# Performance work log

Measured on AMD Instinct MI355X. Metric: run time of the kernel, lower is better.

## Reference

```python
import jax, jax.numpy as jnp
import numpy as np

HEADS = 8
NEG_SLOPE = 0.2


def _gat_conv(x, src, dst, W, a_src, a_dst, b, heads, ch):
    # PyG GATConv (v1), eval mode (dropout inactive), add_self_loops=True, concat=True.
    N = x.shape[0]
    loop = jnp.arange(N)
    s = jnp.concatenate([src, loop])
    d = jnp.concatenate([dst, loop])
    h = (x @ W).reshape(N, heads, ch)                      # [N, H, C]
    alpha_src = jnp.einsum('nhc,hc->nh', h, a_src)          # [N, H]
    alpha_dst = jnp.einsum('nhc,hc->nh', h, a_dst)
    e = jax.nn.leaky_relu(alpha_src[s] + alpha_dst[d], NEG_SLOPE)  # [E, H]
    m = jax.ops.segment_max(e, d, num_segments=N)           # segment softmax over dst
    ex = jnp.exp(e - m[d])
    denom = jax.ops.segment_sum(ex, d, num_segments=N)
    alpha = ex / (denom[d] + 1e-16)
    out = jax.ops.segment_sum(h[s] * alpha[:, :, None], d, num_segments=N)  # [N, H, C]
    return out.reshape(N, heads * ch) + b


def setup_inputs() -> dict:
    key = jax.random.key(0)
    ks = jax.random.split(key, 20)
    B, N, F_in = 8, 1024, 16
    E = 131072
    C1, C2 = 8, 128                     # per-head channels of conv1 / conv2
    D = N * HEADS * C2                  # flattened head input = 1024*1024
    NA, AC = 4, 4                       # len(num_actions)=4, each 4 actions

    def w(k, shape, fan_in):
        return jax.random.normal(k, shape, jnp.float32) * (1.0 / np.sqrt(fan_in))

    inp = {
        'x': jax.random.normal(ks[0], (B, N, F_in), jnp.float32),
        'edge': jax.random.randint(ks[1], (2, E), 0, B * N, jnp.int64),
        'W1': w(ks[2], (F_in, HEADS * C1), F_in),
        'a_src1': w(ks[3], (HEADS, C1), C1),
        'a_dst1': w(ks[4], (HEADS, C1), C1),
        'b1': jnp.zeros((HEADS * C1,), jnp.float32),
        'W2': w(ks[5], (HEADS * C1, HEADS * C2), HEADS * C1),
        'a_src2': w(ks[6], (HEADS, C2), C2),
        'a_dst2': w(ks[7], (HEADS, C2), C2),
        'b2': jnp.zeros((HEADS * C2,), jnp.float32),
        'adv_w': w(ks[8], (D, NA * AC), D),
        'adv_b': jnp.zeros((NA * AC,), jnp.float32),
        'val1_w': w(ks[9], (D, 64), D),
        'val1_b': jnp.zeros((64,), jnp.float32),
        'val2_w': w(ks[10], (64, 64), 64),
        'val2_b': jnp.zeros((64,), jnp.float32),
        'val3_w': w(ks[11], (64, 1), 64),
        'val3_b': jnp.zeros((1,), jnp.float32),
    }
    return inp


def reference(x, edge, W1, a_src1, a_dst1, b1, W2, a_src2, a_dst2, b2,
              adv_w, adv_b, val1_w, val1_b, val2_w, val2_b, val3_w, val3_b):
    B, N, F_in = x.shape
    src, dst = edge[0], edge[1]
    h = x.reshape(B * N, F_in)
    h = jax.nn.relu(_gat_conv(h, src, dst, W1, a_src1, a_dst1, b1, HEADS, 8))
    h = jax.nn.relu(_gat_conv(h, src, dst, W2, a_src2, a_dst2, b2, HEADS, 128))
    h = h.reshape(B, -1)                                   # [B, N*1024]
    adv = jax.nn.relu(h @ adv_w + adv_b).reshape(B, 4, 4)  # [B, len(num_actions), actions]
    v = jax.nn.relu(h @ val1_w + val1_b)
    v = jax.nn.relu(v @ val2_w + val2_b)
    v = v @ val3_w + val3_b                                # [B, 1]
    return v[:, :, None] + adv - adv.mean(-1, keepdims=True)
```

## Files before the change

### kernel.cpp

```cpp
#include <hip/hip_runtime.h>
#include <stdint.h>

#define NODES   8192
#define BATCH   8
#define FIN     16
#define HC1     64
#define HC2     1024
#define DTOT    1048576
#define NEG     0.2f

typedef unsigned short u16;

__device__ __forceinline__ float b2f(u16 s){ return __uint_as_float(((unsigned)s)<<16); }
__device__ __forceinline__ u16 f2b(float f){
    unsigned u = __float_as_uint(f);
    unsigned r = u + 0x7fffu + ((u>>16)&1u);
    return (u16)(r>>16);
}
__device__ __forceinline__ float lrelu(float x){ return x > 0.f ? x : NEG*x; }
__device__ __forceinline__ float ldf(const void* p, long i, int isf){
    return isf ? ((const float*)p)[i] : b2f(((const u16*)p)[i]);
}

__device__ __forceinline__ int esrc(const int* e, int i, int i64){ return i64 ? e[2*i] : e[i]; }
__device__ __forceinline__ int edst(const int* e, int i, int E, int i64){ return i64 ? e[2*(E+i)] : e[E+i]; }

__global__ __launch_bounds__(256) void k_prep(const u16* __restrict__ xs, const int* __restrict__ ed,
        int* flags, int* counts){
    int t = threadIdx.x;
    if(blockIdx.x == 0){
        __shared__ int cnt[2];
        if(t<2) cnt[t]=0;
        __syncthreads();
        int bad=0;
        for(int i=t;i<1024;i+=256){
            u16 u = xs[i];
            float a = fabsf(b2f(u));
            if(!(u==0 || (a>1e-8f && a<1e4f))) bad++;
        }
        if(bad) atomicAdd(&cnt[0], bad);
        int z=0;
        for(int i=t;i<1024;i+=256){
            if(ed[2*i+1]==0) z++;
        }
        if(z) atomicAdd(&cnt[1], z);
        __syncthreads();
        if(t==0){ flags[0] = (cnt[0] > 64) ? 1 : 0; flags[1] = (cnt[1] > 512) ? 1 : 0; }
    } else {
        int i = (blockIdx.x-1)*256 + t;
        if(i < NODES) counts[i] = 0;
    }
}

__global__ __launch_bounds__(256) void k_cnt_d1(const int* __restrict__ ed, int E, int* counts,
        const void* __restrict__ x, const void* __restrict__ W1,
        const void* __restrict__ asw, const void* __restrict__ adw,
        float* g1, float* as1, float* ad1, const int* flags){
    int t = threadIdx.x;
    if(blockIdx.x < 512){
        int i64 = flags[1];
        int e = blockIdx.x*256 + t;
        if(e < E) atomicAdd(&counts[edst(ed,e,E,i64)], 1);
        return;
    }
    int isf = flags[0];
    __shared__ float w1[FIN*HC1];
    __shared__ float av[64], dv[64];
    __shared__ float xr[4][FIN];
    __shared__ float hrow[4][HC1];
    int n0 = (blockIdx.x-512)*4;
    for(int i=t;i<FIN*HC1;i+=256) w1[i] = ldf(W1,i,isf);
    if(t<64){ av[t]=ldf(asw,t,isf); dv[t]=ldf(adw,t,isf); }
    if(t<64) xr[t>>4][t&15] = ldf(x, n0*FIN + t, isf);
    __syncthreads();
    int i = t>>6, c = t&63;
    float acc = 0.f;
    #pragma unroll
    for(int k=0;k<FIN;k++) acc += xr[i][k]*w1[k*HC1+c];
    g1[(n0+i)*HC1 + c] = acc;
    hrow[i][c] = acc;
    __syncthreads();
    if(t<32){
        int ii=t>>3, h=t&7;
        float sa=0.f, sd=0.f;
        #pragma unroll
        for(int k=0;k<8;k++){ float v=hrow[ii][h*8+k]; sa+=v*av[h*8+k]; sd+=v*dv[h*8+k]; }
        as1[(n0+ii)*8+h]=sa; ad1[(n0+ii)*8+h]=sd;
    }
}

__global__ __launch_bounds__(1024) void k_scan(const int* __restrict__ counts, int* offs, int* cursor){
    __shared__ int sums[1024];
    int t = threadIdx.x;
    int base = t*8;
    int loc[8]; int s = 0;
    for(int k=0;k<8;k++){ loc[k] = s; s += counts[base+k]; }
    sums[t] = s;
    __syncthreads();
    for(int off=1; off<1024; off<<=1){
        int v = (t>=off) ? sums[t-off] : 0;
        __syncthreads();
        sums[t] += v;
        __syncthreads();
    }
    int b = (t==0) ? 0 : sums[t-1];
    for(int k=0;k<8;k++){ int v = b + loc[k]; offs[base+k]=v; cursor[base+k]=v; }
    if(t==1023) offs[NODES] = sums[1023];
}

__global__ void k_fill(const int* __restrict__ ed, int E, int* cursor, int* csr, const int* flags){
    int i64 = flags[1];
    int e = blockIdx.x*256 + threadIdx.x;
    if(e < E){ int p = atomicAdd(&cursor[edst(ed,e,E,i64)], 1); csr[p] = esrc(ed,e,i64); }
}

__global__ __launch_bounds__(64) void k_agg1(const int* __restrict__ offs, const int* __restrict__ csr,
        const float* __restrict__ g1, const float* __restrict__ as1, const float* __restrict__ ad1,
        const void* __restrict__ b1, float* z1, const int* flags){
    int isf = flags[0];
    __shared__ float redm[64], redd[64];
    __shared__ float mh[8], dh[8], adl[8];
    __shared__ int src_l[64];
    __shared__ float wx[64*8];
    int n = blockIdx.x, t = threadIdx.x;
    int off = offs[n], deg = offs[n+1]-off, tot = deg+1;
    if(t<8) adl[t] = ad1[n*8+t];
    __syncthreads();
    {
        int h = t&7, jg = t>>3;
        float ad = adl[h];
        float m = -1e30f, d = 0.f;
        for(int j=jg; j<tot; j+=8){
            int s = (j<deg)?csr[off+j]:n;
            float e = lrelu(as1[s*8+h] + ad);
            if(e>m){ d = d*__expf(m-e) + 1.f; m = e; } else d += __expf(e-m);
        }
        redm[t]=m; redd[t]=d;
        __syncthreads();
        for(int st=4; st>=1; st>>=1){
            if(jg < st){
                float m2 = redm[t + st*8], d2 = redd[t + st*8];
                float mm = fmaxf(m, m2);
                d = d*__expf(m-mm) + d2*__expf(m2-mm);
                m = mm;
                redm[t]=m; redd[t]=d;
            }
            __syncthreads();
        }
        if(t<8){ mh[t]=redm[t]; dh[t]=redd[t] + 1e-16f; }
        __syncthreads();
    }
    int c = t, hc = t>>3;
    float acc = 0.f;
    for(int c0=0;c0<tot;c0+=64){
        int nc = min(64, tot-c0);
        if(t<nc){ int j=c0+t; src_l[t]=(j<deg)?csr[off+j]:n; }
        __syncthreads();
        for(int p=t;p<nc*8;p+=64){
            int j=p>>3, hh=p&7;
            float e = lrelu(as1[src_l[j]*8+hh] + adl[hh]);
            wx[p] = __expf(e - mh[hh]);
        }
        __syncthreads();
        int j = 0;
        for(; j+2<=nc; j+=2){
            float w0 = wx[j*8+hc],     v0 = g1[src_l[j]*HC1 + c];
            float w1 = wx[(j+1)*8+hc], v1 = g1[src_l[j+1]*HC1 + c];
            acc += w0*v0 + w1*v1;
        }
        if(j<nc) acc += wx[j*8+hc]*g1[src_l[j]*HC1 + c];
        __syncthreads();
    }
    z1[n*HC1 + c] = fmaxf(acc/dh[hc] + ldf(b1,c,isf), 0.f);
}

__global__ __launch_bounds__(256) void k_d2a2(const float* __restrict__ z1,
        const void* __restrict__ W2, const void* __restrict__ asw, const void* __restrict__ adw,
        u16* g2, float* as2, float* ad2, const int* flags){
    int isf = flags[0];
    __shared__ float zr[8][HC1];
    __shared__ float avs[HC2], ads[HC2];
    int t = threadIdx.x;
    int n0 = blockIdx.x*8;
    for(int i=t;i<8*HC1;i+=256) zr[i>>6][i&63] = z1[n0*HC1 + i];
    for(int i=t;i<HC2;i+=256){ avs[i]=ldf(asw,i,isf); ads[i]=ldf(adw,i,isf); }
    __syncthreads();
    int c0 = t*4;
    float acc[8][4];
    #pragma unroll
    for(int i=0;i<8;i++){ acc[i][0]=0;acc[i][1]=0;acc[i][2]=0;acc[i][3]=0; }
    for(int k=0;k<HC1;k++){
        float w0,w1,w2,w3;
        if(isf){
            float4 w = *(const float4*)((const float*)W2 + (size_t)k*HC2 + c0);
            w0=w.x; w1=w.y; w2=w.z; w3=w.w;
        } else {
            ushort4 w = *(const ushort4*)((const u16*)W2 + (size_t)k*HC2 + c0);
            w0=b2f(w.x); w1=b2f(w.y); w2=b2f(w.z); w3=b2f(w.w);
        }
        #pragma unroll
        for(int i=0;i<8;i++){
            float zv = zr[i][k];
            acc[i][0]+=zv*w0; acc[i][1]+=zv*w1; acc[i][2]+=zv*w2; acc[i][3]+=zv*w3;
        }
    }
    float a0=avs[c0], a1=avs[c0+1], a2=avs[c0+2], a3=avs[c0+3];
    float d0=ads[c0], d1=ads[c0+1], d2=ads[c0+2], d3=ads[c0+3];
    int h = t>>5;
    #pragma unroll
    for(int i=0;i<8;i++){
        ushort4 o;
        o.x=f2b(acc[i][0]); o.y=f2b(acc[i][1]); o.z=f2b(acc[i][2]); o.w=f2b(acc[i][3]);
        *(ushort4*)&g2[(size_t)(n0+i)*HC2 + c0] = o;
        float pa = acc[i][0]*a0 + acc[i][1]*a1 + acc[i][2]*a2 + acc[i][3]*a3;
        float pd = acc[i][0]*d0 + acc[i][1]*d1 + acc[i][2]*d2 + acc[i][3]*d3;
        #pragma unroll
        for(int m=1;m<32;m<<=1){ pa += __shfl_xor(pa,m); pd += __shfl_xor(pd,m); }
        if((t&31)==0){ as2[(n0+i)*8+h]=pa; ad2[(n0+i)*8+h]=pd; }
    }
}

__global__ __launch_bounds__(256) void k_agg2(const int* __restrict__ offs, const int* __restrict__ csr,
        const u16* __restrict__ g2, const float* __restrict__ as2, const float* __restrict__ ad2,
        const void* __restrict__ b2, u16* hbf, const int* flags){
    int isf = flags[0];
    __shared__ float redm[256], redd[256];
    __shared__ float mh[8], dh[8], adl[8];
    __shared__ int src_l[64];
    __shared__ float wx[64*8];
    int n = blockIdx.x, t = threadIdx.x;
    int off = offs[n], deg = offs[n+1]-off, tot = deg+1;
    if(t<8) adl[t] = ad2[n*8+t];
    __syncthreads();
    {
        int h = t&7, jg = t>>3;
        float ad = adl[h];
        float m = -1e30f, d = 0.f;
        for(int j=jg; j<tot; j+=32){
            int s = (j<deg)?csr[off+j]:n;
            float e = lrelu(as2[s*8+h] + ad);
            if(e>m){ d = d*__expf(m-e) + 1.f; m = e; } else d += __expf(e-m);
        }
        redm[t]=m; redd[t]=d;
        __syncthreads();
        for(int st=16; st>=1; st>>=1){
            if(jg < st){
                float m2 = redm[t + st*8], d2 = redd[t + st*8];
                float mm = fmaxf(m, m2);
                d = d*__expf(m-mm) + d2*__expf(m2-mm);
                m = mm;
                redm[t]=m; redd[t]=d;
            }
            __syncthreads();
        }
        if(t<8){ mh[t]=redm[t]; dh[t]=redd[t] + 1e-16f; }
        __syncthreads();
    }
    int c0 = t*4, hc = t>>5;
    float acc[4] = {0,0,0,0};
    for(int cc0=0;cc0<tot;cc0+=64){
        int nc = min(64, tot-cc0);
        if(t<nc){ int j=cc0+t; src_l[t]=(j<deg)?csr[off+j]:n; }
        __syncthreads();
        for(int p=t;p<nc*8;p+=256){
            int j=p>>3, hh=p&7;
            float e = lrelu(as2[src_l[j]*8+hh] + adl[hh]);
            wx[p] = __expf(e - mh[hh]);
        }
        __syncthreads();
        int j = 0;
        for(; j+2<=nc; j+=2){
            float w0 = wx[j*8+hc], w1 = wx[(j+1)*8+hc];
            ushort4 gv0 = *(const ushort4*)&g2[(size_t)src_l[j]*HC2 + c0];
            ushort4 gv1 = *(const ushort4*)&g2[(size_t)src_l[j+1]*HC2 + c0];
            acc[0]+=w0*b2f(gv0.x)+w1*b2f(gv1.x);
            acc[1]+=w0*b2f(gv0.y)+w1*b2f(gv1.y);
            acc[2]+=w0*b2f(gv0.z)+w1*b2f(gv1.z);
            acc[3]+=w0*b2f(gv0.w)+w1*b2f(gv1.w);
        }
        if(j<nc){
            float w = wx[j*8+hc];
            ushort4 gv = *(const ushort4*)&g2[(size_t)src_l[j]*HC2 + c0];
            acc[0]+=w*b2f(gv.x); acc[1]+=w*b2f(gv.y); acc[2]+=w*b2f(gv.z); acc[3]+=w*b2f(gv.w);
        }
        __syncthreads();
    }
    float dhv = dh[hc];
    ushort4 o;
    o.x = f2b(fmaxf(acc[0]/dhv + ldf(b2,c0+0,isf), 0.f));
    o.y = f2b(fmaxf(acc[1]/dhv + ldf(b2,c0+1,isf), 0.f));
    o.z = f2b(fmaxf(acc[2]/dhv + ldf(b2,c0+2,isf), 0.f));
    o.w = f2b(fmaxf(acc[3]/dhv + ldf(b2,c0+3,isf), 0.f));
    *(ushort4*)&hbf[(size_t)n*HC2 + c0] = o;
}

template<int COLS, int NW>
__device__ __forceinline__ void gemv_part(const void* __restrict__ W, const u16* __restrict__ hbf,
        float* __restrict__ scratch, int wid, int lane, int isf){
    const int GR    = COLS/8;
    const int KSTEP = 64/GR;
    const int ITERS = DTOT/(NW*KSTEP);
    int cg  = (lane % GR)*8;
    int kof = lane / GR;
    float acc[8][8];
    #pragma unroll
    for(int b=0;b<8;b++)
        #pragma unroll
        for(int c=0;c<8;c++) acc[b][c]=0.f;
    for(int it=0; it<ITERS; it+=2){
        int k0 = (it*NW + wid)*KSTEP + kof;
        int k1 = ((it+1)*NW + wid)*KSTEP + kof;
        float wv0[8], wv1[8];
        if(isf){
            float4 a0 = *(const float4*)((const float*)W + (size_t)k0*COLS + cg);
            float4 b0 = *(const float4*)((const float*)W + (size_t)k0*COLS + cg + 4);
            float4 a1 = *(const float4*)((const float*)W + (size_t)k1*COLS + cg);
            float4 b1 = *(const float4*)((const float*)W + (size_t)k1*COLS + cg + 4);
            wv0[0]=a0.x;wv0[1]=a0.y;wv0[2]=a0.z;wv0[3]=a0.w;wv0[4]=b0.x;wv0[5]=b0.y;wv0[6]=b0.z;wv0[7]=b0.w;
            wv1[0]=a1.x;wv1[1]=a1.y;wv1[2]=a1.z;wv1[3]=a1.w;wv1[4]=b1.x;wv1[5]=b1.y;wv1[6]=b1.z;wv1[7]=b1.w;
        } else {
            ushort4 a0 = *(const ushort4*)((const u16*)W + (size_t)k0*COLS + cg);
            ushort4 b0 = *(const ushort4*)((const u16*)W + (size_t)k0*COLS + cg + 4);
            ushort4 a1 = *(const ushort4*)((const u16*)W + (size_t)k1*COLS + cg);
            ushort4 b1 = *(const ushort4*)((const u16*)W + (size_t)k1*COLS + cg + 4);
            wv0[0]=b2f(a0.x);wv0[1]=b2f(a0.y);wv0[2]=b2f(a0.z);wv0[3]=b2f(a0.w);
            wv0[4]=b2f(b0.x);wv0[5]=b2f(b0.y);wv0[6]=b2f(b0.z);wv0[7]=b2f(b0.w);
            wv1[0]=b2f(a1.x);wv1[1]=b2f(a1.y);wv1[2]=b2f(a1.z);wv1[3]=b2f(a1.w);
            wv1[4]=b2f(b1.x);wv1[5]=b2f(b1.y);wv1[6]=b2f(b1.z);wv1[7]=b2f(b1.w);
        }
        float hv0[8], hv1[8];
        #pragma unroll
        for(int b=0;b<8;b++){ hv0[b] = b2f(hbf[(size_t)b*DTOT + k0]); hv1[b] = b2f(hbf[(size_t)b*DTOT + k1]); }
        #pragma unroll
        for(int b=0;b<8;b++)
            #pragma unroll
            for(int c=0;c<8;c++) acc[b][c] += hv0[b]*wv0[c] + hv1[b]*wv1[c];
    }
    #pragma unroll
    for(int m=GR;m<64;m<<=1){
        #pragma unroll
        for(int b=0;b<8;b++)
            #pragma unroll
            for(int c=0;c<8;c++) acc[b][c] += __shfl_xor(acc[b][c], m);
    }
    int q = lane / GR;
    if(q < 8){
        float4 o0, o1;
        o0.x=acc[q][0]; o0.y=acc[q][1]; o0.z=acc[q][2]; o0.w=acc[q][3];
        o1.x=acc[q][4]; o1.y=acc[q][5]; o1.z=acc[q][6]; o1.w=acc[q][7];
        float* dst = scratch + (size_t)wid*COLS*8 + q*COLS + cg;
        *(float4*)dst       = o0;
        *(float4*)(dst + 4) = o1;
    }
}

__global__ __launch_bounds__(256) void k_heads(const void* __restrict__ v1w, const void* __restrict__ advw,
        const u16* __restrict__ hbf, float* s1, float* s2, const int* flags){
    int isf = flags[0];
    int lane = threadIdx.x & 63;
    if(blockIdx.x < 1024){
        int wid = (int)((blockIdx.x*256 + threadIdx.x) >> 6);
        gemv_part<64,4096>(v1w, hbf, s1, wid, lane, isf);
    } else {
        int wid = (int)(((blockIdx.x-1024)*256 + threadIdx.x) >> 6);
        gemv_part<16,1024>(advw, hbf, s2, wid, lane, isf);
    }
}

__global__ __launch_bounds__(1024) void k_reduce(const float* __restrict__ s1, const float* __restrict__ s2,
        float* v1a, float* adva){
    __shared__ float red[1024];
    int blk = blockIdx.x, t = threadIdx.x;
    int ph = t>>6, ln = t&63;
    float a = 0.f;
    if(blk < 8){
        int o = blk*64 + ln;
        for(int p = ph; p < 4096; p += 16) a += s1[(size_t)p*512 + o];
        red[t] = a; __syncthreads();
        if(t<64){ float s=0.f; for(int q=0;q<16;q++) s += red[q*64+t]; v1a[blk*64+t]=s; }
    } else {
        int o = (blk-8)*64 + ln;
        for(int p = ph; p < 1024; p += 16) a += s2[(size_t)p*128 + o];
        red[t] = a; __syncthreads();
        if(t<64){ float s=0.f; for(int q=0;q<16;q++) s += red[q*64+t]; adva[(blk-8)*64+t]=s; }
    }
}

__global__ __launch_bounds__(512) void k_final(const float* __restrict__ v1a, const float* __restrict__ adva,
        const void* __restrict__ v1b, const void* __restrict__ advb,
        const void* __restrict__ w2v, const void* __restrict__ b2v,
        const void* __restrict__ w3v, const void* __restrict__ b3v,
        void* out, const int* flags){
    int isf = flags[0];
    __shared__ float v1[8][64], v2[8][64], adv[128], v3[8];
    int t = threadIdx.x;
    { int b=t>>6, j=t&63; v1[b][j] = fmaxf(v1a[t] + ldf(v1b,j,isf), 0.f); }
    if(t<128) adv[t] = fmaxf(adva[t] + ldf(advb,t&15,isf), 0.f);
    __syncthreads();
    { int b=t>>6, j=t&63;
      float a=0.f;
      for(int k=0;k<64;k++) a += v1[b][k]*ldf(w2v,k*64+j,isf);
      v2[b][j] = fmaxf(a + ldf(b2v,j,isf), 0.f); }
    __syncthreads();
    if(t<8){
        float a=0.f;
        for(int k=0;k<64;k++) a += v2[t][k]*ldf(w3v,k,isf);
        v3[t] = a + ldf(b3v,0,isf);
    }
    __syncthreads();
    if(t<128){
        int b=t>>4, r=(t>>2)&3;
        int base = b*16 + r*4;
        float m = 0.25f*(adv[base]+adv[base+1]+adv[base+2]+adv[base+3]);
        float val = v3[b] + adv[t] - m;
        if(isf) ((float*)out)[t] = val;
        else    ((u16*)out)[t]   = f2b(val);
    }
}

extern "C" void kernel_launch(void* const* d_in, const int* in_sizes, int n_in,
                              void* d_out, int out_size, void* d_ws, size_t ws_size,
                              hipStream_t stream){
    const void* x    = d_in[0];
    const int*  edge = (const int*)d_in[1];
    const int E = in_sizes[1]/2;
    const void* W1   = d_in[2];
    const void* as1w = d_in[3];
    const void* ad1w = d_in[4];
    const void* b1   = d_in[5];
    const void* W2   = d_in[6];
    const void* as2w = d_in[7];
    const void* ad2w = d_in[8];
    const void* b2   = d_in[9];
    const void* advw = d_in[10];
    const void* advb = d_in[11];
    const void* v1w  = d_in[12];
    const void* v1b  = d_in[13];
    const void* v2w  = d_in[14];
    const void* v2b  = d_in[15];
    const void* v3w  = d_in[16];
    const void* v3b  = d_in[17];

    char* wsp = (char*)d_ws;
    size_t o = 0;
    auto alloc = [&](size_t bytes)->char*{
        char* p = wsp + o;
        o = (o + bytes + 255) & ~(size_t)255;
        return p;
    };
    int*   flags  = (int*)  alloc(256);
    int*   counts = (int*)  alloc(NODES*4);
    int*   offs   = (int*)  alloc((NODES+8)*4);
    int*   cursor = (int*)  alloc(NODES*4);
    int*   csr    = (int*)  alloc((size_t)E*4);
    float* g1     = (float*)alloc((size_t)NODES*HC1*4);
    float* as1    = (float*)alloc((size_t)NODES*8*4);
    float* ad1    = (float*)alloc((size_t)NODES*8*4);
    float* z1     = (float*)alloc((size_t)NODES*HC1*4);
    u16*   g2     = (u16*)  alloc((size_t)NODES*HC2*2);
    float* as2    = (float*)alloc((size_t)NODES*8*4);
    float* ad2    = (float*)alloc((size_t)NODES*8*4);
    u16*   hbf    = (u16*)  alloc((size_t)NODES*HC2*2);
    float* s1     = (float*)alloc((size_t)4096*512*4);
    float* s2     = (float*)alloc((size_t)1024*128*4);
    float* v1a    = (float*)alloc(512*4);
    float* adva   = (float*)alloc(128*4);

    k_prep  <<<33, 256, 0, stream>>>((const u16*)x, edge, flags, counts);
    k_cnt_d1<<<2560, 256, 0, stream>>>(edge, E, counts, x, W1, as1w, ad1w, g1, as1, ad1, flags);
    k_scan  <<<1, 1024, 0, stream>>>(counts, offs, cursor);
    k_fill  <<<(E+255)/256, 256, 0, stream>>>(edge, E, cursor, csr, flags);
    k_agg1  <<<NODES, 64, 0, stream>>>(offs, csr, g1, as1, ad1, b1, z1, flags);
    k_d2a2  <<<NODES/8, 256, 0, stream>>>(z1, W2, as2w, ad2w, g2, as2, ad2, flags);
    k_agg2  <<<NODES, 256, 0, stream>>>(offs, csr, g2, as2, ad2, b2, hbf, flags);
    k_heads <<<1280, 256, 0, stream>>>(v1w, advw, hbf, s1, s2, flags);
    k_reduce<<<10, 1024, 0, stream>>>(s1, s2, v1a, adva);
    k_final <<<1, 512, 0, stream>>>(v1a, adva, v1b, advb, v2w, v2b, v3w, v3b, d_out, flags);
}
```

Baseline: 681.4 us.

## Reassociate GAT layers to aggregate inputs before projection and fold attention vectors

Both GAT layers now aggregate the narrow per-node inputs (x for layer 1, z1 for layer 2) with the attention weights, then apply the linear projection per head, instead of projecting every node first and gathering the wide projected rows. Attention logits are computed through precomputed products W·a_src and W·a_dst, so the bf16 g2 intermediate of 8192x1024 is never materialised or gathered per edge. The layer-2 aggregation gathers 64-float z1 rows rather than 1024-wide bf16 rows, but writes an 8x64 per-node buffer and moves the W2 GEMM after aggregation. It also fuses CSR fill with the W2·a precompute and fuses the layer-1 projection into aggregation, at the cost of changed rounding order.

New measurement: 749.1 us. 9.9% more time.

```diff
diff --git a/kernel.cpp b/kernel.cpp
--- a/kernel.cpp
+++ b/kernel.cpp
@@ -52,10 +52,10 @@
     }
 }
 
-__global__ __launch_bounds__(256) void k_cnt_d1(const int* __restrict__ ed, int E, int* counts,
+__global__ __launch_bounds__(256) void k_cnt_a1(const int* __restrict__ ed, int E, int* counts,
         const void* __restrict__ x, const void* __restrict__ W1,
         const void* __restrict__ asw, const void* __restrict__ adw,
-        float* g1, float* as1, float* ad1, const int* flags){
+        float* as1, float* ad1, const int* flags){
     int t = threadIdx.x;
     if(blockIdx.x < 512){
         int i64 = flags[1];
@@ -64,28 +64,32 @@
         return;
     }
     int isf = flags[0];
-    __shared__ float w1[FIN*HC1];
-    __shared__ float av[64], dv[64];
-    __shared__ float xr[4][FIN];
-    __shared__ float hrow[4][HC1];
-    int n0 = (blockIdx.x-512)*4;
-    for(int i=t;i<FIN*HC1;i+=256) w1[i] = ldf(W1,i,isf);
-    if(t<64){ av[t]=ldf(asw,t,isf); dv[t]=ldf(adw,t,isf); }
-    if(t<64) xr[t>>4][t&15] = ldf(x, n0*FIN + t, isf);
-    __syncthreads();
-    int i = t>>6, c = t&63;
-    float acc = 0.f;
-    #pragma unroll
-    for(int k=0;k<FIN;k++) acc += xr[i][k]*w1[k*HC1+c];
-    g1[(n0+i)*HC1 + c] = acc;
-    hrow[i][c] = acc;
-    __syncthreads();
-    if(t<32){
-        int ii=t>>3, h=t&7;
-        float sa=0.f, sd=0.f;
-        #pragma unroll
-        for(int k=0;k<8;k++){ float v=hrow[ii][h*8+k]; sa+=v*av[h*8+k]; sd+=v*dv[h*8+k]; }
-        as1[(n0+ii)*8+h]=sa; ad1[(n0+ii)*8+h]=sd;
+    __shared__ float w1l[FIN*HC1];
+    __shared__ float p1[2][FIN][8];
+    __shared__ float xl[128][FIN];
+    int n0 = (blockIdx.x-512)*128;
+    for(int q=0;q<4;q++) w1l[t + q*256] = ldf(W1, t + q*256, isf);
+    for(int q=0;q<8;q++){ int f = t + q*256; xl[f>>4][f&15] = ldf(x, (long)n0*FIN + f, isf); }
+    __syncthreads();
+    {
+        int sd = t>>7, k = (t>>3)&15, h = t&7;
+        const void* av = sd ? adw : asw;
+        float s = 0.f;
+        #pragma unroll
+        for(int c=0;c<8;c++) s += w1l[k*HC1 + h*8 + c] * ldf(av, h*8+c, isf);
+        p1[sd][k][h] = s;
+    }
+    __syncthreads();
+    {
+        int i = t>>1, sd = t&1;
+        float* outp = sd ? ad1 : as1;
+        #pragma unroll
+        for(int h=0;h<8;h++){
+            float s = 0.f;
+            #pragma unroll
+            for(int k=0;k<FIN;k++) s += xl[i][k] * p1[sd][k][h];
+            outp[(size_t)(n0+i)*8 + h] = s;
+        }
     }
 }
 
@@ -108,22 +112,43 @@
     if(t==1023) offs[NODES] = sums[1023];
 }
 
-__global__ void k_fill(const int* __restrict__ ed, int E, int* cursor, int* csr, const int* flags){
-    int i64 = flags[1];
-    int e = blockIdx.x*256 + threadIdx.x;
-    if(e < E){ int p = atomicAdd(&cursor[edst(ed,e,E,i64)], 1); csr[p] = esrc(ed,e,i64); }
-}
-
-__global__ __launch_bounds__(64) void k_agg1(const int* __restrict__ offs, const int* __restrict__ csr,
-        const float* __restrict__ g1, const float* __restrict__ as1, const float* __restrict__ ad1,
-        const void* __restrict__ b1, float* z1, const int* flags){
+__global__ __launch_bounds__(256) void k_fill_p2(const int* __restrict__ ed, int E, int* cursor, int* csr,
+        const void* __restrict__ W2, const void* __restrict__ asw2, const void* __restrict__ adw2,
+        float* p2s, float* p2d, const int* flags){
+    int t = threadIdx.x;
+    if(blockIdx.x < 512){
+        int i64 = flags[1];
+        int e = blockIdx.x*256 + t;
+        if(e < E){ int p = atomicAdd(&cursor[edst(ed,e,E,i64)], 1); csr[p] = esrc(ed,e,i64); }
+        return;
+    }
     int isf = flags[0];
+    for(int q=0;q<4;q++){
+        int task = t + q*256;
+        int sd = task>>9, k = (task>>3)&63, h = task&7;
+        const void* av = sd ? adw2 : asw2;
+        float s = 0.f;
+        for(int c=0;c<128;c++) s += ldf(W2, (long)k*HC2 + h*128 + c, isf) * ldf(av, h*128+c, isf);
+        (sd ? p2d : p2s)[k*8 + h] = s;
+    }
+}
+
+__global__ __launch_bounds__(64) void k_l1(const int* __restrict__ offs, const int* __restrict__ csr,
+        const void* __restrict__ x, const void* __restrict__ W1, const void* __restrict__ b1,
+        const float* __restrict__ as1, const float* __restrict__ ad1,
+        const float* __restrict__ p2s, const float* __restrict__ p2d,
+        float* z1, float* as2, float* ad2, const int* flags){
+    int isf = flags[0];
+    __shared__ float w1l[FIN*HC1];
     __shared__ float redm[64], redd[64];
     __shared__ float mh[8], dh[8], adl[8];
     __shared__ int src_l[64];
     __shared__ float wx[64*8];
+    __shared__ float aggx[8][FIN];
+    __shared__ float zl[HC1];
     int n = blockIdx.x, t = threadIdx.x;
     int off = offs[n], deg = offs[n+1]-off, tot = deg+1;
+    for(int q=0;q<16;q++) w1l[t + q*64] = ldf(W1, t + q*64, isf);
     if(t<8) adl[t] = ad1[n*8+t];
     __syncthreads();
     {
@@ -150,8 +175,8 @@
         if(t<8){ mh[t]=redm[t]; dh[t]=redd[t] + 1e-16f; }
         __syncthreads();
     }
-    int c = t, hc = t>>3;
-    float acc = 0.f;
+    int c = t&15, hq = t>>4;
+    float acc0 = 0.f, acc1 = 0.f;
     for(int c0=0;c0<tot;c0+=64){
         int nc = min(64, tot-c0);
         if(t<nc){ int j=c0+t; src_l[t]=(j<deg)?csr[off+j]:n; }
@@ -164,28 +189,122 @@
         __syncthreads();
         int j = 0;
         for(; j+2<=nc; j+=2){
-            float w0 = wx[j*8+hc],     v0 = g1[src_l[j]*HC1 + c];
-            float w1 = wx[(j+1)*8+hc], v1 = g1[src_l[j+1]*HC1 + c];
-            acc += w0*v0 + w1*v1;
-        }
-        if(j<nc) acc += wx[j*8+hc]*g1[src_l[j]*HC1 + c];
-        __syncthreads();
-    }
-    z1[n*HC1 + c] = fmaxf(acc/dh[hc] + ldf(b1,c,isf), 0.f);
-}
-
-__global__ __launch_bounds__(256) void k_d2a2(const float* __restrict__ z1,
-        const void* __restrict__ W2, const void* __restrict__ asw, const void* __restrict__ adw,
-        u16* g2, float* as2, float* ad2, const int* flags){
+            float x0 = ldf(x, (long)src_l[j]*FIN + c, isf);
+            float x1 = ldf(x, (long)src_l[j+1]*FIN + c, isf);
+            acc0 += wx[j*8+hq]*x0     + wx[(j+1)*8+hq]*x1;
+            acc1 += wx[j*8+hq+4]*x0   + wx[(j+1)*8+hq+4]*x1;
+        }
+        if(j<nc){
+            float x0 = ldf(x, (long)src_l[j]*FIN + c, isf);
+            acc0 += wx[j*8+hq]*x0;
+            acc1 += wx[j*8+hq+4]*x0;
+        }
+        __syncthreads();
+    }
+    aggx[hq][c]   = acc0/dh[hq];
+    aggx[hq+4][c] = acc1/dh[hq+4];
+    __syncthreads();
+    {
+        int h = t>>3;
+        float s = 0.f;
+        #pragma unroll
+        for(int k=0;k<FIN;k++) s += aggx[h][k]*w1l[k*HC1 + t];
+        float zv = fmaxf(s + ldf(b1, t, isf), 0.f);
+        z1[(size_t)n*HC1 + t] = zv;
+        zl[t] = zv;
+    }
+    __syncthreads();
+    if(t<8){
+        float s = 0.f;
+        for(int k=0;k<HC1;k++) s += zl[k]*p2s[k*8+t];
+        as2[n*8+t] = s;
+    } else if(t<16){
+        int tt = t-8;
+        float s = 0.f;
+        for(int k=0;k<HC1;k++) s += zl[k]*p2d[k*8+tt];
+        ad2[n*8+tt] = s;
+    }
+}
+
+__global__ __launch_bounds__(64) void k_aggz(const int* __restrict__ offs, const int* __restrict__ csr,
+        const float* __restrict__ z1, const float* __restrict__ as2, const float* __restrict__ ad2,
+        float* aggz){
+    __shared__ float redm[64], redd[64];
+    __shared__ float mh[8], dh[8], adl[8];
+    __shared__ int src_l[64];
+    __shared__ float wx[64*8];
+    int n = blockIdx.x, t = threadIdx.x;
+    int off = offs[n], deg = offs[n+1]-off, tot = deg+1;
+    if(t<8) adl[t] = ad2[n*8+t];
+    __syncthreads();
+    {
+        int h = t&7, jg = t>>3;
+        float ad = adl[h];
+        float m = -1e30f, d = 0.f;
+        for(int j=jg; j<tot; j+=8){
+            int s = (j<deg)?csr[off+j]:n;
+            float e = lrelu(as2[s*8+h] + ad);
+            if(e>m){ d = d*__expf(m-e) + 1.f; m = e; } else d += __expf(e-m);
+        }
+        redm[t]=m; redd[t]=d;
+        __syncthreads();
+        for(int st=4; st>=1; st>>=1){
+            if(jg < st){
+                float m2 = redm[t + st*8], d2 = redd[t + st*8];
+                float mm = fmaxf(m, m2);
+                d = d*__expf(m-mm) + d2*__expf(m2-mm);
+                m = mm;
+                redm[t]=m; redd[t]=d;
+            }
+            __syncthreads();
+        }
+        if(t<8){ mh[t]=redm[t]; dh[t]=redd[t] + 1e-16f; }
+        __syncthreads();
+    }
+    float acc[8];
+    #pragma unroll
+    for(int h=0;h<8;h++) acc[h]=0.f;
+    for(int c0=0;c0<tot;c0+=64){
+        int nc = min(64, tot-c0);
+        if(t<nc){ int j=c0+t; src_l[t]=(j<deg)?csr[off+j]:n; }
+        __syncthreads();
+        for(int p=t;p<nc*8;p+=64){
+            int j=p>>3, hh=p&7;
+            float e = lrelu(as2[src_l[j]*8+hh] + adl[hh]);
+            wx[p] = __expf(e - mh[hh]);
+        }
+        __syncthreads();
+        int j = 0;
+        for(; j+2<=nc; j+=2){
+            float z0 = z1[(size_t)src_l[j]*HC1 + t];
+            float z1v = z1[(size_t)src_l[j+1]*HC1 + t];
+            #pragma unroll
+            for(int h=0;h<8;h++) acc[h] += wx[j*8+h]*z0 + wx[(j+1)*8+h]*z1v;
+        }
+        if(j<nc){
+            float z0 = z1[(size_t)src_l[j]*HC1 + t];
+            #pragma unroll
+            for(int h=0;h<8;h++) acc[h] += wx[j*8+h]*z0;
+        }
+        __syncthreads();
+    }
+    #pragma unroll
+    for(int h=0;h<8;h++)
+        aggz[((size_t)n*8 + h)*HC1 + t] = acc[h]/dh[h];
+}
+
+__global__ __launch_bounds__(256) void k_d2(const float* __restrict__ aggz,
+        const void* __restrict__ W2, const void* __restrict__ b2, u16* hbf, const int* flags){
     int isf = flags[0];
-    __shared__ float zr[8][HC1];
-    __shared__ float avs[HC2], ads[HC2];
+    __shared__ float az[8][512];
     int t = threadIdx.x;
     int n0 = blockIdx.x*8;
-    for(int i=t;i<8*HC1;i+=256) zr[i>>6][i&63] = z1[n0*HC1 + i];
-    for(int i=t;i<HC2;i+=256){ avs[i]=ldf(asw,i,isf); ads[i]=ldf(adw,i,isf); }
-    __syncthreads();
-    int c0 = t*4;
+    for(int q=0;q<16;q++){
+        int f = t + q*256;
+        az[f>>9][f&511] = aggz[(size_t)n0*512 + f];
+    }
+    __syncthreads();
+    int c0 = t*4, h = t>>5;
     float acc[8][4];
     #pragma unroll
     for(int i=0;i<8;i++){ acc[i][0]=0;acc[i][1]=0;acc[i][2]=0;acc[i][3]=0; }
@@ -200,98 +319,20 @@
         }
         #pragma unroll
         for(int i=0;i<8;i++){
-            float zv = zr[i][k];
+            float zv = az[i][h*64 + k];
             acc[i][0]+=zv*w0; acc[i][1]+=zv*w1; acc[i][2]+=zv*w2; acc[i][3]+=zv*w3;
         }
     }
-    float a0=avs[c0], a1=avs[c0+1], a2=avs[c0+2], a3=avs[c0+3];
-    float d0=ads[c0], d1=ads[c0+1], d2=ads[c0+2], d3=ads[c0+3];
-    int h = t>>5;
+    float bb0 = ldf(b2,c0+0,isf), bb1 = ldf(b2,c0+1,isf), bb2 = ldf(b2,c0+2,isf), bb3 = ldf(b2,c0+3,isf);
     #pragma unroll
     for(int i=0;i<8;i++){
         ushort4 o;
-        o.x=f2b(acc[i][0]); o.y=f2b(acc[i][1]); o.z=f2b(acc[i][2]); o.w=f2b(acc[i][3]);
-        *(ushort4*)&g2[(size_t)(n0+i)*HC2 + c0] = o;
-        float pa = acc[i][0]*a0 + acc[i][1]*a1 + acc[i][2]*a2 + acc[i][3]*a3;
-        float pd = acc[i][0]*d0 + acc[i][1]*d1 + acc[i][2]*d2 + acc[i][3]*d3;
-        #pragma unroll
-        for(int m=1;m<32;m<<=1){ pa += __shfl_xor(pa,m); pd += __shfl_xor(pd,m); }
-        if((t&31)==0){ as2[(n0+i)*8+h]=pa; ad2[(n0+i)*8+h]=pd; }
-    }
-}
-
-__global__ __launch_bounds__(256) void k_agg2(const int* __restrict__ offs, const int* __restrict__ csr,
-        const u16* __restrict__ g2, const float* __restrict__ as2, const float* __restrict__ ad2,
-        const void* __restrict__ b2, u16* hbf, const int* flags){
-    int isf = flags[0];
-    __shared__ float redm[256], redd[256];
-    __shared__ float mh[8], dh[8], adl[8];
-    __shared__ int src_l[64];
-    __shared__ float wx[64*8];
-    int n = blockIdx.x, t = threadIdx.x;
-    int off = offs[n], deg = offs[n+1]-off, tot = deg+1;
-    if(t<8) adl[t] = ad2[n*8+t];
-    __syncthreads();
-    {
-        int h = t&7, jg = t>>3;
-        float ad = adl[h];
-        float m = -1e30f, d = 0.f;
-        for(int j=jg; j<tot; j+=32){
-            int s = (j<deg)?csr[off+j]:n;
-            float e = lrelu(as2[s*8+h] + ad);
-            if(e>m){ d = d*__expf(m-e) + 1.f; m = e; } else d += __expf(e-m);
-        }
-        redm[t]=m; redd[t]=d;
-        __syncthreads();
-        for(int st=16; st>=1; st>>=1){
-            if(jg < st){
-                float m2 = redm[t + st*8], d2 = redd[t + st*8];
-                float mm = fmaxf(m, m2);
-                d = d*__expf(m-mm) + d2*__expf(m2-mm);
-                m = mm;
-                redm[t]=m; redd[t]=d;
-            }
-            __syncthreads();
-        }
-        if(t<8){ mh[t]=redm[t]; dh[t]=redd[t] + 1e-16f; }
-        __syncthreads();
-    }
-    int c0 = t*4, hc = t>>5;
-    float acc[4] = {0,0,0,0};
-    for(int cc0=0;cc0<tot;cc0+=64){
-        int nc = min(64, tot-cc0);
-        if(t<nc){ int j=cc0+t; src_l[t]=(j<deg)?csr[off+j]:n; }
-        __syncthreads();
-        for(int p=t;p<nc*8;p+=256){
-            int j=p>>3, hh=p&7;
-            float e = lrelu(as2[src_l[j]*8+hh] + adl[hh]);
-            wx[p] = __expf(e - mh[hh]);
-        }
-        __syncthreads();
-        int j = 0;
-        for(; j+2<=nc; j+=2){
-            float w0 = wx[j*8+hc], w1 = wx[(j+1)*8+hc];
-            ushort4 gv0 = *(const ushort4*)&g2[(size_t)src_l[j]*HC2 + c0];
-            ushort4 gv1 = *(const ushort4*)&g2[(size_t)src_l[j+1]*HC2 + c0];
-            acc[0]+=w0*b2f(gv0.x)+w1*b2f(gv1.x);
-            acc[1]+=w0*b2f(gv0.y)+w1*b2f(gv1.y);
-            acc[2]+=w0*b2f(gv0.z)+w1*b2f(gv1.z);
-            acc[3]+=w0*b2f(gv0.w)+w1*b2f(gv1.w);
-        }
-        if(j<nc){
-            float w = wx[j*8+hc];
-            ushort4 gv = *(const ushort4*)&g2[(size_t)src_l[j]*HC2 + c0];
-            acc[0]+=w*b2f(gv.x); acc[1]+=w*b2f(gv.y); acc[2]+=w*b2f(gv.z); acc[3]+=w*b2f(gv.w);
-        }
-        __syncthreads();
-    }
-    float dhv = dh[hc];
-    ushort4 o;
-    o.x = f2b(fmaxf(acc[0]/dhv + ldf(b2,c0+0,isf), 0.f));
-    o.y = f2b(fmaxf(acc[1]/dhv + ldf(b2,c0+1,isf), 0.f));
-    o.z = f2b(fmaxf(acc[2]/dhv + ldf(b2,c0+2,isf), 0.f));
-    o.w = f2b(fmaxf(acc[3]/dhv + ldf(b2,c0+3,isf), 0.f));
-    *(ushort4*)&hbf[(size_t)n*HC2 + c0] = o;
+        o.x=f2b(fmaxf(acc[i][0]+bb0, 0.f));
+        o.y=f2b(fmaxf(acc[i][1]+bb1, 0.f));
+        o.z=f2b(fmaxf(acc[i][2]+bb2, 0.f));
+        o.w=f2b(fmaxf(acc[i][3]+bb3, 0.f));
+        *(ushort4*)&hbf[(size_t)(n0+i)*HC2 + c0] = o;
+    }
 }
 
 template<int COLS, int NW>
@@ -453,27 +494,28 @@
     int*   offs   = (int*)  alloc((NODES+8)*4);
     int*   cursor = (int*)  alloc(NODES*4);
     int*   csr    = (int*)  alloc((size_t)E*4);
-    float* g1     = (float*)alloc((size_t)NODES*HC1*4);
     float* as1    = (float*)alloc((size_t)NODES*8*4);
     float* ad1    = (float*)alloc((size_t)NODES*8*4);
     float* z1     = (float*)alloc((size_t)NODES*HC1*4);
-    u16*   g2     = (u16*)  alloc((size_t)NODES*HC2*2);
     float* as2    = (float*)alloc((size_t)NODES*8*4);
     float* ad2    = (float*)alloc((size_t)NODES*8*4);
+    float* p2s    = (float*)alloc(HC1*8*4);
+    float* p2d    = (float*)alloc(HC1*8*4);
+    float* aggz   = (float*)alloc((size_t)NODES*8*HC1*4);
     u16*   hbf    = (u16*)  alloc((size_t)NODES*HC2*2);
     float* s1     = (float*)alloc((size_t)4096*512*4);
     float* s2     = (float*)alloc((size_t)1024*128*4);
     float* v1a    = (float*)alloc(512*4);
     float* adva   = (float*)alloc(128*4);
 
-    k_prep  <<<33, 256, 0, stream>>>((const u16*)x, edge, flags, counts);
-    k_cnt_d1<<<2560, 256, 0, stream>>>(edge, E, counts, x, W1, as1w, ad1w, g1, as1, ad1, flags);
-    k_scan  <<<1, 1024, 0, stream>>>(counts, offs, cursor);
-    k_fill  <<<(E+255)/256, 256, 0, stream>>>(edge, E, cursor, csr, flags);
-    k_agg1  <<<NODES, 64, 0, stream>>>(offs, csr, g1, as1, ad1, b1, z1, flags);
-    k_d2a2  <<<NODES/8, 256, 0, stream>>>(z1, W2, as2w, ad2w, g2, as2, ad2, flags);
-    k_agg2  <<<NODES, 256, 0, stream>>>(offs, csr, g2, as2, ad2, b2, hbf, flags);
-    k_heads <<<1280, 256, 0, stream>>>(v1w, advw, hbf, s1, s2, flags);
-    k_reduce<<<10, 1024, 0, stream>>>(s1, s2, v1a, adva);
-    k_final <<<1, 512, 0, stream>>>(v1a, adva, v1b, advb, v2w, v2b, v3w, v3b, d_out, flags);
-}
+    k_prep   <<<33, 256, 0, stream>>>((const u16*)x, edge, flags, counts);
+    k_cnt_a1 <<<576, 256, 0, stream>>>(edge, E, counts, x, W1, as1w, ad1w, as1, ad1, flags);
+    k_scan   <<<1, 1024, 0, stream>>>(counts, offs, cursor);
+    k_fill_p2<<<513, 256, 0, stream>>>(edge, E, cursor, csr, W2, as2w, ad2w, p2s, p2d, flags);
+    k_l1     <<<NODES, 64, 0, stream>>>(offs, csr, x, W1, b1, as1, ad1, p2s, p2d, z1, as2, ad2, flags);
+    k_aggz   <<<NODES, 64, 0, stream>>>(offs, csr, z1, as2, ad2, aggz);
+    k_d2     <<<NODES/8, 256, 0, stream>>>(aggz, W2, b2, hbf, flags);
+    k_heads  <<<1280, 256, 0, stream>>>(v1w, advw, hbf, s1, s2, flags);
+    k_reduce <<<10, 1024, 0, stream>>>(s1, s2, v1a, adva);
+    k_final  <<<1, 512, 0, stream>>>(v1a, adva, v1b, advb, v2w, v2b, v3w, v3b, d_out, flags);
+}
```
